# Optimization experiments

Measured on AMD Instinct MI355X. Metric: run time of the kernel, lower is better.

## Reference

```python
import jax, jax.numpy as jnp
import numpy as np

D_MODEL = 1024
N_HEADS = 16
D_HEAD = D_MODEL // N_HEADS
LUT_SIZE = 4096
TWO_PI = 2.0 * np.pi
SCALE = np.sqrt(2.0 * D_HEAD).astype(np.float32)

# Global sin/cos lookup table over [0, 2*pi), 4096 entries (mirrors get_global_lut(4096)).
_GRID = (TWO_PI * np.arange(LUT_SIZE) / LUT_SIZE).astype(np.float32)
_SIN_TABLE = jnp.asarray(np.sin(_GRID))
_COS_TABLE = jnp.asarray(np.cos(_GRID))


def _lut_sin_cos(theta):
    # quantize angle to nearest LUT bin (wrap mod 2*pi) and gather
    idx = jnp.mod(jnp.round(theta * (LUT_SIZE / TWO_PI)).astype(jnp.int32), LUT_SIZE)
    return _SIN_TABLE[idx], _COS_TABLE[idx]


def setup_inputs() -> dict:
    key = jax.random.key(0)
    ks = jax.random.split(key, 7)
    B, S = 2, 2048
    x = jax.random.normal(ks[0], (B, S, D_MODEL), dtype=jnp.float32)
    w_q = 0.02 * jax.random.normal(ks[1], (N_HEADS, D_HEAD), dtype=jnp.float32)
    b_q = jnp.zeros((N_HEADS, D_HEAD), dtype=jnp.float32)
    w_k = 0.02 * jax.random.normal(ks[2], (N_HEADS, D_HEAD), dtype=jnp.float32)
    b_k = jnp.zeros((N_HEADS, D_HEAD), dtype=jnp.float32)
    v_w = jax.random.normal(ks[3], (D_MODEL, D_MODEL), dtype=jnp.float32) / np.sqrt(D_MODEL)
    out_w = jax.random.normal(ks[4], (D_MODEL, D_MODEL), dtype=jnp.float32) / np.sqrt(D_MODEL)
    return {"x": x, "w_q": w_q, "b_q": b_q, "w_k": w_k, "b_k": b_k, "v_w": v_w, "out_w": out_w}


def reference(x, w_q, b_q, w_k, b_k, v_w, out_w):
    B, S, D = x.shape
    x_heads = x.reshape(B, S, N_HEADS, D_HEAD)

    theta_q = x_heads / (1.0 + jnp.abs(w_q)) + b_q          # (B,S,H,dh)
    sin_q, cos_q = _lut_sin_cos(theta_q)
    Q = jnp.concatenate([cos_q, sin_q], axis=-1)            # (B,S,H,2dh)

    theta_k = x_heads / (1.0 + jnp.abs(w_k)) + b_k
    sin_k, cos_k = _lut_sin_cos(theta_k)
    K = jnp.concatenate([cos_k, sin_k], axis=-1)            # (B,S,H,2dh)

    V = (x @ v_w.T).reshape(B, S, N_HEADS, D_HEAD)          # (B,S,H,dh)

    scores = jnp.einsum("bqhe,bkhe->bhqk", Q, K) / SCALE    # (B,H,S,S)
    causal = jnp.triu(jnp.ones((S, S), dtype=bool), k=1)
    scores = jnp.where(causal, -jnp.inf, scores)
    attn = jax.nn.softmax(scores, axis=-1)

    out = jnp.einsum("bhqk,bkhd->bqhd", attn, V).reshape(B, S, D)
    return out @ out_w.T
```

## Files before the change

kernel.cpp:

```cpp
#include <hip/hip_runtime.h>
#include <hip/hip_bf16.h>
#include <math.h>


typedef __attribute__((ext_vector_type(8))) __bf16 bf16x8;
typedef __attribute__((ext_vector_type(4))) __bf16 bf16x4;
typedef __attribute__((ext_vector_type(4))) float f32x4;
typedef unsigned short ushort_t;
typedef unsigned int uint_t;

#define LUTC 651.8986469044033f
#define ANG 0.0015339807878856412f
#define QSCL 0.12751743590489435f

__device__ __forceinline__ float fast_exp2(float x) {
#if __has_builtin(__builtin_amdgcn_exp2f)
  return __builtin_amdgcn_exp2f(x);
#else
  return exp2f(x);
#endif
}

__device__ __forceinline__ ushort_t f2bf(float f) {
  union { __bf16 b; ushort_t u; } cv;
  cv.b = (__bf16)f;
  return cv.u;
}

__device__ __forceinline__ void store8(ushort_t* p, const ushort_t v[8]) {
  uint4 u;
  u.x = (uint_t)v[0] | ((uint_t)v[1] << 16);
  u.y = (uint_t)v[2] | ((uint_t)v[3] << 16);
  u.z = (uint_t)v[4] | ((uint_t)v[5] << 16);
  u.w = (uint_t)v[6] | ((uint_t)v[7] << 16);
  *(uint4*)p = u;
}

__device__ __forceinline__ void gl_lds16(const void* g, void* l) {
  __builtin_amdgcn_global_load_lds(
      (__attribute__((address_space(1))) void*)(g),
      (__attribute__((address_space(3))) void*)(l),
      16, 0, 0);
}

__global__ __launch_bounds__(256) void prep_kernel(
    const float* __restrict__ x, const float* __restrict__ wq, const float* __restrict__ bq,
    const float* __restrict__ wk, const float* __restrict__ bk,
    ushort_t* __restrict__ Qs, ushort_t* __restrict__ Ks, ushort_t* __restrict__ xb)
{
  int t = blockIdx.x * 256 + threadIdx.x;
  int dm8 = t & 127;
  int g = t >> 7;
  int dm0 = dm8 * 8;
  int h = dm0 >> 6;

  float aq[8], cq[8], ak[8], ck[8];
#pragma unroll
  for (int j = 0; j < 8; ++j) {
    aq[j] = LUTC / (1.0f + fabsf(wq[dm0 + j]));
    cq[j] = LUTC * bq[dm0 + j];
    ak[j] = LUTC / (1.0f + fabsf(wk[dm0 + j]));
    ck[j] = LUTC * bk[dm0 + j];
  }
  for (int i = 0; i < 4; ++i) {
    int bs = g * 4 + i;
    int b = bs >> 11, s = bs & 2047;
    const float4* xp4 = (const float4*)(x + (size_t)bs * 1024 + dm0);
    float4 xa = xp4[0], xbv4 = xp4[1];
    float xv[8] = {xa.x, xa.y, xa.z, xa.w, xbv4.x, xbv4.y, xbv4.z, xbv4.w};
    ushort_t qc[8], qs[8], kc[8], ks[8], xo[8];
#pragma unroll
    for (int j = 0; j < 8; ++j) {
      int iq = ((int)rintf(fmaf(xv[j], aq[j], cq[j]))) & 4095;
      float sq, cqv;
      __sincosf((float)iq * ANG, &sq, &cqv);
      int ik = ((int)rintf(fmaf(xv[j], ak[j], ck[j]))) & 4095;
      float sk, ckv;
      __sincosf((float)ik * ANG, &sk, &ckv);
      qc[j] = f2bf(cqv * QSCL);
      qs[j] = f2bf(sq * QSCL);
      kc[j] = f2bf(ckv);
      ks[j] = f2bf(sk);
      xo[j] = f2bf(xv[j]);
    }
    size_t qb = ((size_t)(b * 16 + h) * 2048 + s) * 128 + (dm0 & 63);
    store8(Qs + qb, qc);        store8(Qs + qb + 64, qs);
    store8(Ks + qb, kc);        store8(Ks + qb + 64, ks);
    store8(xb + (size_t)bs * 1024 + dm0, xo);
  }
}

__global__ __launch_bounds__(256) void wconv_kernel(
    const float* __restrict__ vw, const float* __restrict__ ow,
    ushort_t* __restrict__ vwb, ushort_t* __restrict__ owb)
{
  int t = blockIdx.x * 256 + threadIdx.x;
  const float* src;
  ushort_t* dst;
  int i;
  if (t < 131072) { src = vw; dst = vwb; i = t; }
  else            { src = ow; dst = owb; i = t - 131072; }
  const float4* p4 = (const float4*)(src + (size_t)i * 8);
  float4 a = p4[0], b = p4[1];
  float v[8] = {a.x, a.y, a.z, a.w, b.x, b.y, b.z, b.w};
  ushort_t o[8];
#pragma unroll
  for (int j = 0; j < 8; ++j) o[j] = f2bf(v[j]);
  store8(dst + (size_t)i * 8, o);
}

template <int EPI>
__global__ __launch_bounds__(256) void gemm_nt(
    const ushort_t* __restrict__ A, const ushort_t* __restrict__ B,
    float* __restrict__ Cf, ushort_t* __restrict__ Cb, int M, int N, int K)
{
  __shared__ __align__(16) ushort_t As[2][64 * 64];
  __shared__ __align__(16) ushort_t Bs[2][128 * 64];
  const int l = threadIdx.x & 63;
  const int w = threadIdx.x >> 6;
  const int g = l >> 4, lo = l & 15;
  const int mt = blockIdx.x % (M >> 6);
  const int nt = blockIdx.x / (M >> 6);
  const int m0 = mt << 6, n0 = nt << 7;

  const f32x4 zero4 = {0.f, 0.f, 0.f, 0.f};
  f32x4 acc[4][2];
#pragma unroll
  for (int i = 0; i < 4; ++i)
#pragma unroll
    for (int j = 0; j < 2; ++j) acc[i][j] = zero4;

  const int nk = K >> 6;

#define GEMM_STAGE(buf, k0_)                                                    \
  {                                                                             \
    int k0__ = (k0_);                                                           \
    _Pragma("unroll")                                                           \
    for (int i = 0; i < 2; ++i) {                                               \
      int ci = (w * 2 + i) * 64 + l;                                            \
      int r = ci >> 3, c = (ci & 7) ^ (r & 7);                                  \
      gl_lds16(A + (size_t)(m0 + r) * K + k0__ + c * 8, &As[buf][(w * 2 + i) * 512]); \
    }                                                                           \
    _Pragma("unroll")                                                           \
    for (int i = 0; i < 4; ++i) {                                               \
      int ci = (w * 4 + i) * 64 + l;                                            \
      int r = ci >> 3, c = (ci & 7) ^ (r & 7);                                  \
      gl_lds16(B + (size_t)(n0 + r) * K + k0__ + c * 8, &Bs[buf][(w * 4 + i) * 512]); \
    }                                                                           \
  }

  GEMM_STAGE(0, 0);
  GEMM_STAGE(1, 64);
  asm volatile("s_waitcnt vmcnt(6)" ::: "memory");
  __builtin_amdgcn_s_barrier();
  __builtin_amdgcn_sched_barrier(0);

  for (int t = 0; t < nk; ++t) {
    int cb = t & 1;
#pragma unroll
    for (int kk = 0; kk < 2; ++kk) {
      bf16x8 af[4], bfr[2];
#pragma unroll
      for (int mi = 0; mi < 4; ++mi) {
        int r = mi * 16 + lo;
        int ch = (g + 4 * kk) ^ (r & 7);
        af[mi] = *(const bf16x8*)&As[cb][r * 64 + ch * 8];
      }
#pragma unroll
      for (int ni = 0; ni < 2; ++ni) {
        int r = w * 32 + ni * 16 + lo;
        int ch = (g + 4 * kk) ^ (r & 7);
        bfr[ni] = *(const bf16x8*)&Bs[cb][r * 64 + ch * 8];
      }
#pragma unroll
      for (int mi = 0; mi < 4; ++mi)
#pragma unroll
        for (int ni = 0; ni < 2; ++ni)
          acc[mi][ni] = __builtin_amdgcn_mfma_f32_16x16x32_bf16(af[mi], bfr[ni], acc[mi][ni], 0, 0, 0);
    }
    __builtin_amdgcn_sched_barrier(0);
    asm volatile("s_waitcnt lgkmcnt(0)" ::: "memory");
    __builtin_amdgcn_s_barrier();
    if (t + 2 < nk) {
      GEMM_STAGE(cb, (t + 2) * 64);
      asm volatile("s_waitcnt vmcnt(6)" ::: "memory");
    } else {
      asm volatile("s_waitcnt vmcnt(0)" ::: "memory");
    }
    __builtin_amdgcn_s_barrier();
    __builtin_amdgcn_sched_barrier(0);
  }
#undef GEMM_STAGE

#pragma unroll
  for (int mi = 0; mi < 4; ++mi)
#pragma unroll
    for (int ni = 0; ni < 2; ++ni)
#pragma unroll
      for (int reg = 0; reg < 4; ++reg) {
        int row = m0 + mi * 16 + g * 4 + reg;
        int col = n0 + w * 32 + ni * 16 + lo;
        float v = acc[mi][ni][reg];
        if (EPI == 0) {
          Cf[(size_t)row * N + col] = v;
        } else {
          size_t o = (size_t)(col >> 11) * (1024 * 2048) + (size_t)row * 2048 + (col & 2047);
          Cb[o] = f2bf(v);
        }
      }
}


template<bool MASKED>
__device__ __forceinline__ void attn_step_kh(
    const ushort_t* __restrict__ Kc, const ushort_t* __restrict__ Vc,
    const bf16x8 (&qf)[4][4], f32x4 (&accO)[4][4], f32x4 (&acc_l)[4],
    int kb_glob, int q0, int lo, int g, const bf16x8& ones)
{
  const f32x4 zero4 = {0.f, 0.f, 0.f, 0.f};
  bf16x8 pa[4];
#pragma unroll
  for (int ns = 0; ns < 2; ++ns) {
    f32x4 sc[4];
#pragma unroll
    for (int qm = 0; qm < 4; ++qm) sc[qm] = zero4;
#pragma unroll
    for (int e = 0; e < 4; ++e) {
      int kr = ns * 16 + lo;
      int cc = (g + 4 * e) ^ (kr & 7);
      bf16x8 kf = *(const bf16x8*)&Kc[kr * 128 + cc * 8];
#pragma unroll
      for (int qm = 0; qm < 4; ++qm)
        sc[qm] = __builtin_amdgcn_mfma_f32_16x16x32_bf16(kf, qf[qm][e], sc[qm], 0, 0, 0);
    }
#pragma unroll
    for (int qm = 0; qm < 4; ++qm) {
#pragma unroll
      for (int reg = 0; reg < 4; ++reg) {
        float sv = sc[qm][reg];
        if (MASKED) {
          int ka = kb_glob + ns * 16 + 4 * g + reg;
          int qa = q0 + qm * 16 + lo;
          sv = (ka <= qa) ? sv : -__builtin_inff();
        }
        pa[qm][ns * 4 + reg] = (__bf16)fast_exp2(sv);
      }
    }
  }
#pragma unroll
  for (int nd = 0; nd < 4; ++nd) {
    int vr = nd * 16 + lo;
    int h8 = (g & 1) * 4;
    int cc0 = ((g >> 1)) ^ (vr & 3);
    int cc1 = (2 + (g >> 1)) ^ (vr & 3);
    union { bf16x8 v8; bf16x4 v4[2]; } u;
    u.v4[0] = *(const bf16x4*)&Vc[vr * 32 + cc0 * 8 + h8];
    u.v4[1] = *(const bf16x4*)&Vc[vr * 32 + cc1 * 8 + h8];
#pragma unroll
    for (int qm = 0; qm < 4; ++qm)
      accO[qm][nd] = __builtin_amdgcn_mfma_f32_16x16x32_bf16(pa[qm], u.v8, accO[qm][nd], 0, 0, 0);
  }
#pragma unroll
  for (int qm = 0; qm < 4; ++qm)
    acc_l[qm] = __builtin_amdgcn_mfma_f32_16x16x32_bf16(pa[qm], ones, acc_l[qm], 0, 0, 0);
}

__global__ __launch_bounds__(128) void attn_kernel(
    const ushort_t* __restrict__ Qs, const ushort_t* __restrict__ Ks,
    const ushort_t* __restrict__ Vt, ushort_t* __restrict__ Ob)
{
  const int S = 2048;
  const int id = blockIdx.x;
  const int bh = id & 31;
  const int qv = 31 - (id >> 5);
  const int nt = qv + 1;
  const int q0 = qv * 64;

  const int l = threadIdx.x & 63;
  const int kh = threadIdx.x >> 6;
  const int g = l >> 4, lo = l & 15;

  __shared__ __align__(16) ushort_t Lds[2][2][4096 + 2048];
  ushort_t* Kw[2] = {&Lds[kh][0][0], &Lds[kh][1][0]};
  ushort_t* Vw[2] = {&Lds[kh][0][4096], &Lds[kh][1][4096]};

  const ushort_t* Kbase = Ks + (size_t)bh * S * 128;
  const ushort_t* Vbase = Vt + (size_t)bh * 64 * S;

  bf16x8 ones;
#pragma unroll
  for (int j = 0; j < 8; ++j) ones[j] = (__bf16)1.0f;

  bf16x8 qf[4][4];
#pragma unroll
  for (int qm = 0; qm < 4; ++qm) {
    const ushort_t* qp = Qs + ((size_t)bh * S + q0 + qm * 16 + lo) * 128 + 8 * g;
#pragma unroll
    for (int e = 0; e < 4; ++e) qf[qm][e] = *(const bf16x8*)(qp + 32 * e);
  }

  const f32x4 zero4 = {0.f, 0.f, 0.f, 0.f};
  f32x4 accO[4][4];
  f32x4 acc_l[4];
#pragma unroll
  for (int qm = 0; qm < 4; ++qm) {
    acc_l[qm] = zero4;
#pragma unroll
    for (int nd = 0; nd < 4; ++nd) accO[qm][nd] = zero4;
  }

#define ATTN_STAGE(buf, kb_)                                                    \
  {                                                                             \
    int kb__ = (kb_) + kh * 32;                                                 \
    _Pragma("unroll")                                                           \
    for (int i = 0; i < 8; ++i) {                                               \
      int ci = i * 64 + l;                                                      \
      int r = ci >> 4, c = (ci & 15) ^ (r & 7);                                 \
      gl_lds16(Kbase + (size_t)(kb__ + r) * 128 + c * 8, Kw[buf] + (size_t)(i * 64) * 8); \
    }                                                                           \
    _Pragma("unroll")                                                           \
    for (int i = 0; i < 4; ++i) {                                               \
      int ci = i * 64 + l;                                                      \
      int r = ci >> 2, c = (ci & 3) ^ (r & 3);                                  \
      gl_lds16(Vbase + (size_t)r * S + kb__ + c * 8, Vw[buf] + (size_t)(i * 64) * 8); \
    }                                                                           \
  }

  ATTN_STAGE(0, 0);
  if (nt > 1) {
    ATTN_STAGE(1, 64);
    asm volatile("s_waitcnt vmcnt(12)" ::: "memory");
  } else {
    asm volatile("s_waitcnt vmcnt(0)" ::: "memory");
  }
  __builtin_amdgcn_sched_barrier(0);

  for (int t = 0; t < nt; ++t) {
    int cb = t & 1;
    if (t < nt - 1)
      attn_step_kh<false>(Kw[cb], Vw[cb], qf, accO, acc_l, t * 64 + kh * 32, q0, lo, g, ones);
    else
      attn_step_kh<true>(Kw[cb], Vw[cb], qf, accO, acc_l, t * 64 + kh * 32, q0, lo, g, ones);
    if (t + 1 < nt) {
      __builtin_amdgcn_sched_barrier(0);
      asm volatile("s_waitcnt lgkmcnt(0)" ::: "memory");
      if (t + 2 < nt) {
        ATTN_STAGE(cb, (t + 2) * 64);
        asm volatile("s_waitcnt vmcnt(12)" ::: "memory");
      } else {
        asm volatile("s_waitcnt vmcnt(0)" ::: "memory");
      }
      __builtin_amdgcn_sched_barrier(0);
    }
  }
#undef ATTN_STAGE

  asm volatile("s_waitcnt vmcnt(0) lgkmcnt(0)" ::: "memory");
  __builtin_amdgcn_s_barrier();
  float* cmb = (float*)&Lds[0][0][0];
  if (kh == 1) {
#pragma unroll
    for (int qm = 0; qm < 4; ++qm) {
#pragma unroll
      for (int nd = 0; nd < 4; ++nd)
#pragma unroll
        for (int reg = 0; reg < 4; ++reg)
          cmb[l * 68 + qm * 16 + nd * 4 + reg] = accO[qm][nd][reg];
#pragma unroll
      for (int reg = 0; reg < 4; ++reg)
        cmb[l * 68 + 64 + qm] = acc_l[qm][0];
    }
#pragma unroll
    for (int qm = 0; qm < 4; ++qm)
#pragma unroll
      for (int reg = 0; reg < 4; ++reg)
        cmb[l * 68 + 64 + 0] = cmb[l * 68 + 64 + 0];
  }
  __builtin_amdgcn_s_barrier();
  float* cmbl = (float*)&Lds[1][0][0];
  if (kh == 1) {
#pragma unroll
    for (int qm = 0; qm < 4; ++qm)
#pragma unroll
      for (int reg = 0; reg < 4; ++reg)
        cmbl[l * 16 + qm * 4 + reg] = acc_l[qm][reg];
  }
  asm volatile("s_waitcnt lgkmcnt(0)" ::: "memory");
  __builtin_amdgcn_s_barrier();

  if (kh == 0) {
#pragma unroll
    for (int qm = 0; qm < 4; ++qm) {
#pragma unroll
      for (int nd = 0; nd < 4; ++nd)
#pragma unroll
        for (int reg = 0; reg < 4; ++reg)
          accO[qm][nd][reg] += cmb[l * 68 + qm * 16 + nd * 4 + reg];
#pragma unroll
      for (int reg = 0; reg < 4; ++reg)
        acc_l[qm][reg] += cmbl[l * 16 + qm * 4 + reg];
    }
    float linv[4][4];
#pragma unroll
    for (int qm = 0; qm < 4; ++qm)
#pragma unroll
      for (int reg = 0; reg < 4; ++reg)
        linv[qm][reg] = 1.0f / acc_l[qm][reg];

    const int b = bh >> 4, h = bh & 15;
#pragma unroll
    for (int qm = 0; qm < 4; ++qm)
#pragma unroll
      for (int nd = 0; nd < 4; ++nd)
#pragma unroll
        for (int reg = 0; reg < 4; ++reg) {
          int q = q0 + qm * 16 + g * 4 + reg;
          int d = nd * 16 + lo;
          Ob[((size_t)(b * 2048 + q)) * 1024 + h * 64 + d] =
              f2bf(accO[qm][nd][reg] * linv[qm][reg]);
        }
  }
}

extern "C" void kernel_launch(void* const* d_in, const int* in_sizes, int n_in,
                              void* d_out, int out_size, void* d_ws, size_t ws_size,
                              hipStream_t stream) {
  const float* x  = (const float*)d_in[0];
  const float* wq = (const float*)d_in[1];
  const float* bq = (const float*)d_in[2];
  const float* wk = (const float*)d_in[3];
  const float* bk = (const float*)d_in[4];
  const float* vw = (const float*)d_in[5];
  const float* ow = (const float*)d_in[6];
  float* out = (float*)d_out;

  char* ws = (char*)d_ws;
  ushort_t* Qs  = (ushort_t*)(ws);
  ushort_t* Ksb = (ushort_t*)(ws + (16u << 20));
  ushort_t* Vtb = (ushort_t*)(ws + (32u << 20));
  ushort_t* xbb = (ushort_t*)(ws + (40u << 20));
  ushort_t* Obb = (ushort_t*)(ws + (48u << 20));
  ushort_t* vwb = (ushort_t*)(ws + (56u << 20));
  ushort_t* owb = (ushort_t*)(ws + (58u << 20));

  prep_kernel<<<512, 256, 0, stream>>>(x, wq, bq, wk, bk, Qs, Ksb, xbb);
  wconv_kernel<<<1024, 256, 0, stream>>>(vw, ow, vwb, owb);
  gemm_nt<1><<<512, 256, 0, stream>>>(vwb, xbb, nullptr, Vtb, 1024, 4096, 1024);
  attn_kernel<<<1024, 128, 0, stream>>>(Qs, Ksb, Vtb, Obb);
  gemm_nt<0><<<512, 256, 0, stream>>>(Obb, owb, out, nullptr, 4096, 1024, 1024);
}
```

Baseline: 112.5 us.

## Merge weight conversion into prep, triple-buffer GEMM, split attention keys across four waves

Folds the weight bf16 conversion into the prep kernel as extra blocks, removing one launch. The GEMM moves to a three-slot LDS ring so the next stage can be issued without the barrier before it. The attention kernel goes from two waves each taking 32 keys per tile to four waves each taking 16, with a half-zero-padded PV MFMA, s_setprio around the compute, and a four-way LDS reduction at the end. The padding wastes half of the PV MFMA work, and the reduction adds more barriers.

```diff
diff --git a/kernel.cpp b/kernel.cpp
--- a/kernel.cpp
+++ b/kernel.cpp
@@ -46,8 +46,27 @@
 __global__ __launch_bounds__(256) void prep_kernel(
     const float* __restrict__ x, const float* __restrict__ wq, const float* __restrict__ bq,
     const float* __restrict__ wk, const float* __restrict__ bk,
-    ushort_t* __restrict__ Qs, ushort_t* __restrict__ Ks, ushort_t* __restrict__ xb)
+    ushort_t* __restrict__ Qs, ushort_t* __restrict__ Ks, ushort_t* __restrict__ xb,
+    const float* __restrict__ vw, const float* __restrict__ ow,
+    ushort_t* __restrict__ vwb, ushort_t* __restrict__ owb)
 {
+  if (blockIdx.x >= 512) {
+    int t = (blockIdx.x - 512) * 256 + threadIdx.x;
+    const float* src;
+    ushort_t* dst;
+    int i;
+    if (t < 131072) { src = vw; dst = vwb; i = t; }
+    else            { src = ow; dst = owb; i = t - 131072; }
+    const float4* p4 = (const float4*)(src + (size_t)i * 8);
+    float4 a = p4[0], b = p4[1];
+    float v[8] = {a.x, a.y, a.z, a.w, b.x, b.y, b.z, b.w};
+    ushort_t o[8];
+#pragma unroll
+    for (int j = 0; j < 8; ++j) o[j] = f2bf(v[j]);
+    store8(dst + (size_t)i * 8, o);
+    return;
+  }
+
   int t = blockIdx.x * 256 + threadIdx.x;
   int dm8 = t & 127;
   int g = t >> 7;
@@ -90,32 +109,13 @@
   }
 }
 
-__global__ __launch_bounds__(256) void wconv_kernel(
-    const float* __restrict__ vw, const float* __restrict__ ow,
-    ushort_t* __restrict__ vwb, ushort_t* __restrict__ owb)
-{
-  int t = blockIdx.x * 256 + threadIdx.x;
-  const float* src;
-  ushort_t* dst;
-  int i;
-  if (t < 131072) { src = vw; dst = vwb; i = t; }
-  else            { src = ow; dst = owb; i = t - 131072; }
-  const float4* p4 = (const float4*)(src + (size_t)i * 8);
-  float4 a = p4[0], b = p4[1];
-  float v[8] = {a.x, a.y, a.z, a.w, b.x, b.y, b.z, b.w};
-  ushort_t o[8];
-#pragma unroll
-  for (int j = 0; j < 8; ++j) o[j] = f2bf(v[j]);
-  store8(dst + (size_t)i * 8, o);
-}
-
 template <int EPI>
 __global__ __launch_bounds__(256) void gemm_nt(
     const ushort_t* __restrict__ A, const ushort_t* __restrict__ B,
     float* __restrict__ Cf, ushort_t* __restrict__ Cb, int M, int N, int K)
 {
-  __shared__ __align__(16) ushort_t As[2][64 * 64];
-  __shared__ __align__(16) ushort_t Bs[2][128 * 64];
+  __shared__ __align__(16) ushort_t As[3][64 * 64];
+  __shared__ __align__(16) ushort_t Bs[3][128 * 64];
   const int l = threadIdx.x & 63;
   const int w = threadIdx.x >> 6;
   const int g = l >> 4, lo = l & 15;
@@ -155,8 +155,8 @@
   __builtin_amdgcn_s_barrier();
   __builtin_amdgcn_sched_barrier(0);
 
+  int rb = 0, wb = 2;
   for (int t = 0; t < nk; ++t) {
-    int cb = t & 1;
 #pragma unroll
     for (int kk = 0; kk < 2; ++kk) {
       bf16x8 af[4], bfr[2];
@@ -164,13 +164,13 @@
       for (int mi = 0; mi < 4; ++mi) {
         int r = mi * 16 + lo;
         int ch = (g + 4 * kk) ^ (r & 7);
-        af[mi] = *(const bf16x8*)&As[cb][r * 64 + ch * 8];
+        af[mi] = *(const bf16x8*)&As[rb][r * 64 + ch * 8];
       }
 #pragma unroll
       for (int ni = 0; ni < 2; ++ni) {
         int r = w * 32 + ni * 16 + lo;
         int ch = (g + 4 * kk) ^ (r & 7);
-        bfr[ni] = *(const bf16x8*)&Bs[cb][r * 64 + ch * 8];
+        bfr[ni] = *(const bf16x8*)&Bs[rb][r * 64 + ch * 8];
       }
 #pragma unroll
       for (int mi = 0; mi < 4; ++mi)
@@ -179,16 +179,20 @@
           acc[mi][ni] = __builtin_amdgcn_mfma_f32_16x16x32_bf16(af[mi], bfr[ni], acc[mi][ni], 0, 0, 0);
     }
     __builtin_amdgcn_sched_barrier(0);
-    asm volatile("s_waitcnt lgkmcnt(0)" ::: "memory");
-    __builtin_amdgcn_s_barrier();
     if (t + 2 < nk) {
-      GEMM_STAGE(cb, (t + 2) * 64);
+      GEMM_STAGE(wb, (t + 2) * 64);
+      asm volatile("s_waitcnt lgkmcnt(0)" ::: "memory");
       asm volatile("s_waitcnt vmcnt(6)" ::: "memory");
-    } else {
+    } else if (t + 1 < nk) {
+      asm volatile("s_waitcnt lgkmcnt(0)" ::: "memory");
       asm volatile("s_waitcnt vmcnt(0)" ::: "memory");
     }
-    __builtin_amdgcn_s_barrier();
-    __builtin_amdgcn_sched_barrier(0);
+    if (t + 1 < nk) {
+      __builtin_amdgcn_s_barrier();
+      __builtin_amdgcn_sched_barrier(0);
+    }
+    rb = (rb == 2) ? 0 : rb + 1;
+    wb = (wb == 2) ? 0 : wb + 1;
   }
 #undef GEMM_STAGE
 
@@ -211,61 +215,7 @@
 }
 
 
-template<bool MASKED>
-__device__ __forceinline__ void attn_step_kh(
-    const ushort_t* __restrict__ Kc, const ushort_t* __restrict__ Vc,
-    const bf16x8 (&qf)[4][4], f32x4 (&accO)[4][4], f32x4 (&acc_l)[4],
-    int kb_glob, int q0, int lo, int g, const bf16x8& ones)
-{
-  const f32x4 zero4 = {0.f, 0.f, 0.f, 0.f};
-  bf16x8 pa[4];
-#pragma unroll
-  for (int ns = 0; ns < 2; ++ns) {
-    f32x4 sc[4];
-#pragma unroll
-    for (int qm = 0; qm < 4; ++qm) sc[qm] = zero4;
-#pragma unroll
-    for (int e = 0; e < 4; ++e) {
-      int kr = ns * 16 + lo;
-      int cc = (g + 4 * e) ^ (kr & 7);
-      bf16x8 kf = *(const bf16x8*)&Kc[kr * 128 + cc * 8];
-#pragma unroll
-      for (int qm = 0; qm < 4; ++qm)
-        sc[qm] = __builtin_amdgcn_mfma_f32_16x16x32_bf16(kf, qf[qm][e], sc[qm], 0, 0, 0);
-    }
-#pragma unroll
-    for (int qm = 0; qm < 4; ++qm) {
-#pragma unroll
-      for (int reg = 0; reg < 4; ++reg) {
-        float sv = sc[qm][reg];
-        if (MASKED) {
-          int ka = kb_glob + ns * 16 + 4 * g + reg;
-          int qa = q0 + qm * 16 + lo;
-          sv = (ka <= qa) ? sv : -__builtin_inff();
-        }
-        pa[qm][ns * 4 + reg] = (__bf16)fast_exp2(sv);
-      }
-    }
-  }
-#pragma unroll
-  for (int nd = 0; nd < 4; ++nd) {
-    int vr = nd * 16 + lo;
-    int h8 = (g & 1) * 4;
-    int cc0 = ((g >> 1)) ^ (vr & 3);
-    int cc1 = (2 + (g >> 1)) ^ (vr & 3);
-    union { bf16x8 v8; bf16x4 v4[2]; } u;
-    u.v4[0] = *(const bf16x4*)&Vc[vr * 32 + cc0 * 8 + h8];
-    u.v4[1] = *(const bf16x4*)&Vc[vr * 32 + cc1 * 8 + h8];
-#pragma unroll
-    for (int qm = 0; qm < 4; ++qm)
-      accO[qm][nd] = __builtin_amdgcn_mfma_f32_16x16x32_bf16(pa[qm], u.v8, accO[qm][nd], 0, 0, 0);
-  }
-#pragma unroll
-  for (int qm = 0; qm < 4; ++qm)
-    acc_l[qm] = __builtin_amdgcn_mfma_f32_16x16x32_bf16(pa[qm], ones, acc_l[qm], 0, 0, 0);
-}
-
-__global__ __launch_bounds__(128) void attn_kernel(
+__global__ __launch_bounds__(256) void attn_kernel(
     const ushort_t* __restrict__ Qs, const ushort_t* __restrict__ Ks,
     const ushort_t* __restrict__ Vt, ushort_t* __restrict__ Ob)
 {
@@ -277,19 +227,13 @@
   const int q0 = qv * 64;
 
   const int l = threadIdx.x & 63;
-  const int kh = threadIdx.x >> 6;
+  const int w = threadIdx.x >> 6;
   const int g = l >> 4, lo = l & 15;
 
-  __shared__ __align__(16) ushort_t Lds[2][2][4096 + 2048];
-  ushort_t* Kw[2] = {&Lds[kh][0][0], &Lds[kh][1][0]};
-  ushort_t* Vw[2] = {&Lds[kh][0][4096], &Lds[kh][1][4096]};
+  __shared__ __align__(16) ushort_t Sh[2][4][3072];
 
   const ushort_t* Kbase = Ks + (size_t)bh * S * 128;
   const ushort_t* Vbase = Vt + (size_t)bh * 64 * S;
-
-  bf16x8 ones;
-#pragma unroll
-  for (int j = 0; j < 8; ++j) ones[j] = (__bf16)1.0f;
 
   bf16x8 qf[4][4];
 #pragma unroll
@@ -309,44 +253,93 @@
     for (int nd = 0; nd < 4; ++nd) accO[qm][nd] = zero4;
   }
 
-#define ATTN_STAGE(buf, kb_)                                                    \
-  {                                                                             \
-    int kb__ = (kb_) + kh * 32;                                                 \
-    _Pragma("unroll")                                                           \
-    for (int i = 0; i < 8; ++i) {                                               \
-      int ci = i * 64 + l;                                                      \
-      int r = ci >> 4, c = (ci & 15) ^ (r & 7);                                 \
-      gl_lds16(Kbase + (size_t)(kb__ + r) * 128 + c * 8, Kw[buf] + (size_t)(i * 64) * 8); \
-    }                                                                           \
-    _Pragma("unroll")                                                           \
-    for (int i = 0; i < 4; ++i) {                                               \
-      int ci = i * 64 + l;                                                      \
-      int r = ci >> 2, c = (ci & 3) ^ (r & 3);                                  \
-      gl_lds16(Vbase + (size_t)r * S + kb__ + c * 8, Vw[buf] + (size_t)(i * 64) * 8); \
-    }                                                                           \
+  bf16x8 ones;
+#pragma unroll
+  for (int j = 0; j < 8; ++j) ones[j] = (__bf16)1.0f;
+
+#define ATTN_STAGE(buf, kb_)                                                      \
+  {                                                                               \
+    int ks__ = (kb_) + w * 16;                                                    \
+    _Pragma("unroll")                                                             \
+    for (int i = 0; i < 4; ++i) {                                                 \
+      int ci = i * 64 + l;                                                        \
+      int r = ci >> 4, c = (ci & 15) ^ (r & 7);                                   \
+      gl_lds16(Kbase + (size_t)(ks__ + r) * 128 + c * 8, &Sh[buf][w][i * 512]);   \
+    }                                                                             \
+    _Pragma("unroll")                                                             \
+    for (int i = 0; i < 2; ++i) {                                                 \
+      int ci = i * 64 + l;                                                        \
+      int d = ci >> 1, c = (ci & 1) ^ (d & 1);                                    \
+      gl_lds16(Vbase + (size_t)d * S + ks__ + c * 8, &Sh[buf][w][2048 + i * 512]); \
+    }                                                                             \
   }
 
   ATTN_STAGE(0, 0);
   if (nt > 1) {
     ATTN_STAGE(1, 64);
-    asm volatile("s_waitcnt vmcnt(12)" ::: "memory");
+    asm volatile("s_waitcnt vmcnt(6)" ::: "memory");
   } else {
     asm volatile("s_waitcnt vmcnt(0)" ::: "memory");
   }
   __builtin_amdgcn_sched_barrier(0);
 
   for (int t = 0; t < nt; ++t) {
-    int cb = t & 1;
-    if (t < nt - 1)
-      attn_step_kh<false>(Kw[cb], Vw[cb], qf, accO, acc_l, t * 64 + kh * 32, q0, lo, g, ones);
-    else
-      attn_step_kh<true>(Kw[cb], Vw[cb], qf, accO, acc_l, t * 64 + kh * 32, q0, lo, g, ones);
+    const ushort_t* Kw = &Sh[t & 1][w][0];
+    const ushort_t* Vw = &Sh[t & 1][w][2048];
+    const bool masked = (t == nt - 1);
+    const int kb = t * 64 + w * 16;
+
+    __builtin_amdgcn_s_setprio(1);
+    f32x4 sc[4];
+#pragma unroll
+    for (int qm = 0; qm < 4; ++qm) sc[qm] = zero4;
+#pragma unroll
+    for (int e = 0; e < 4; ++e) {
+      int cc = (g + 4 * e) ^ (lo & 7);
+      bf16x8 kf = *(const bf16x8*)&Kw[lo * 128 + cc * 8];
+#pragma unroll
+      for (int qm = 0; qm < 4; ++qm)
+        sc[qm] = __builtin_amdgcn_mfma_f32_16x16x32_bf16(kf, qf[qm][e], sc[qm], 0, 0, 0);
+    }
+    bf16x8 pa[4];
+#pragma unroll
+    for (int qm = 0; qm < 4; ++qm) {
+#pragma unroll
+      for (int reg = 0; reg < 4; ++reg) {
+        float sv = sc[qm][reg];
+        if (masked) {
+          int ka = kb + g * 4 + reg;
+          int qa = q0 + qm * 16 + lo;
+          sv = (ka <= qa) ? sv : -__builtin_inff();
+        }
+        pa[qm][reg] = (__bf16)fast_exp2(sv);
+      }
+#pragma unroll
+      for (int reg = 4; reg < 8; ++reg) pa[qm][reg] = (__bf16)0.0f;
+    }
+#pragma unroll
+    for (int nd = 0; nd < 4; ++nd) {
+      int d = nd * 16 + lo;
+      int sg = (g >> 1) ^ (d & 1);
+      bf16x4 v4 = *(const bf16x4*)&Vw[d * 16 + sg * 8 + (g & 1) * 4];
+      bf16x8 vb;
+#pragma unroll
+      for (int j = 0; j < 4; ++j) { vb[j] = v4[j]; vb[4 + j] = (__bf16)0.0f; }
+#pragma unroll
+      for (int qm = 0; qm < 4; ++qm)
+        accO[qm][nd] = __builtin_amdgcn_mfma_f32_16x16x32_bf16(pa[qm], vb, accO[qm][nd], 0, 0, 0);
+    }
+#pragma unroll
+    for (int qm = 0; qm < 4; ++qm)
+      acc_l[qm] = __builtin_amdgcn_mfma_f32_16x16x32_bf16(pa[qm], ones, acc_l[qm], 0, 0, 0);
+    __builtin_amdgcn_s_setprio(0);
+    __builtin_amdgcn_sched_barrier(0);
+
     if (t + 1 < nt) {
-      __builtin_amdgcn_sched_barrier(0);
       asm volatile("s_waitcnt lgkmcnt(0)" ::: "memory");
       if (t + 2 < nt) {
-        ATTN_STAGE(cb, (t + 2) * 64);
-        asm volatile("s_waitcnt vmcnt(12)" ::: "memory");
+        ATTN_STAGE(t & 1, (t + 2) * 64);
+        asm volatile("s_waitcnt vmcnt(6)" ::: "memory");
       } else {
         asm volatile("s_waitcnt vmcnt(0)" ::: "memory");
       }
@@ -355,51 +348,46 @@
   }
 #undef ATTN_STAGE
 
-  asm volatile("s_waitcnt vmcnt(0) lgkmcnt(0)" ::: "memory");
-  __builtin_amdgcn_s_barrier();
-  float* cmb = (float*)&Lds[0][0][0];
-  if (kh == 1) {
-#pragma unroll
-    for (int qm = 0; qm < 4; ++qm) {
+  __syncthreads();
+  float* red = (float*)&Sh[0][0][0];
+  if (w > 0) {
+#pragma unroll
+    for (int qm = 0; qm < 4; ++qm)
 #pragma unroll
       for (int nd = 0; nd < 4; ++nd)
 #pragma unroll
         for (int reg = 0; reg < 4; ++reg)
-          cmb[l * 68 + qm * 16 + nd * 4 + reg] = accO[qm][nd][reg];
+          red[(qm * 16 + nd * 4 + reg) * 192 + (w - 1) * 64 + l] = accO[qm][nd][reg];
+  }
+  __syncthreads();
+  if (w == 0) {
+#pragma unroll
+    for (int qm = 0; qm < 4; ++qm)
+#pragma unroll
+      for (int nd = 0; nd < 4; ++nd)
+#pragma unroll
+        for (int reg = 0; reg < 4; ++reg) {
+          int idx = qm * 16 + nd * 4 + reg;
+          accO[qm][nd][reg] += red[idx * 192 + l] + red[idx * 192 + 64 + l] + red[idx * 192 + 128 + l];
+        }
+  }
+  __syncthreads();
+  if (w > 0) {
+#pragma unroll
+    for (int qm = 0; qm < 4; ++qm)
 #pragma unroll
       for (int reg = 0; reg < 4; ++reg)
-        cmb[l * 68 + 64 + qm] = acc_l[qm][0];
-    }
-#pragma unroll
-    for (int qm = 0; qm < 4; ++qm)
-#pragma unroll
-      for (int reg = 0; reg < 4; ++reg)
-        cmb[l * 68 + 64 + 0] = cmb[l * 68 + 64 + 0];
-  }
-  __builtin_amdgcn_s_barrier();
-  float* cmbl = (float*)&Lds[1][0][0];
-  if (kh == 1) {
-#pragma unroll
-    for (int qm = 0; qm < 4; ++qm)
-#pragma unroll
-      for (int reg = 0; reg < 4; ++reg)
-        cmbl[l * 16 + qm * 4 + reg] = acc_l[qm][reg];
-  }
-  asm volatile("s_waitcnt lgkmcnt(0)" ::: "memory");
-  __builtin_amdgcn_s_barrier();
-
-  if (kh == 0) {
-#pragma unroll
-    for (int qm = 0; qm < 4; ++qm) {
-#pragma unroll
-      for (int nd = 0; nd < 4; ++nd)
-#pragma unroll
-        for (int reg = 0; reg < 4; ++reg)
-          accO[qm][nd][reg] += cmb[l * 68 + qm * 16 + nd * 4 + reg];
-#pragma unroll
-      for (int reg = 0; reg < 4; ++reg)
-        acc_l[qm][reg] += cmbl[l * 16 + qm * 4 + reg];
-    }
+        red[(qm * 4 + reg) * 192 + (w - 1) * 64 + l] = acc_l[qm][reg];
+  }
+  __syncthreads();
+  if (w == 0) {
+#pragma unroll
+    for (int qm = 0; qm < 4; ++qm)
+#pragma unroll
+      for (int reg = 0; reg < 4; ++reg) {
+        int idx = qm * 4 + reg;
+        acc_l[qm][reg] += red[idx * 192 + l] + red[idx * 192 + 64 + l] + red[idx * 192 + 128 + l];
+      }
     float linv[4][4];
 #pragma unroll
     for (int qm = 0; qm < 4; ++qm)
@@ -443,9 +431,9 @@
   ushort_t* vwb = (ushort_t*)(ws + (56u << 20));
   ushort_t* owb = (ushort_t*)(ws + (58u << 20));
 
-  prep_kernel<<<512, 256, 0, stream>>>(x, wq, bq, wk, bk, Qs, Ksb, xbb);
-  wconv_kernel<<<1024, 256, 0, stream>>>(vw, ow, vwb, owb);
+  prep_kernel<<<1536, 256, 0, stream>>>(x, wq, bq, wk, bk, Qs, Ksb, xbb,
+                                        vw, ow, vwb, owb);
   gemm_nt<1><<<512, 256, 0, stream>>>(vwb, xbb, nullptr, Vtb, 1024, 4096, 1024);
-  attn_kernel<<<1024, 128, 0, stream>>>(Qs, Ksb, Vtb, Obb);
+  attn_kernel<<<1024, 256, 0, stream>>>(Qs, Ksb, Vtb, Obb);
   gemm_nt<0><<<512, 256, 0, stream>>>(Obb, owb, out, nullptr, 4096, 1024, 1024);
 }
```

Measured after the change: 99.20 us. -11.8%, faster.
